# Performance work log

Hardware: AMD Instinct MI355X
Metric: run time of the kernel (lower is better)

## Reference

```python
import jax, jax.numpy as jnp
import numpy as np

B, IN, T, E, S, K, W, HD = 4096, 512, 10, 16, 2, 4, 1024, 64


def setup_inputs() -> dict:
    key = jax.random.key(0)
    ks = jax.random.split(key, 12)
    he = lambda k, shp, fan: jax.random.normal(k, shp, jnp.float32) * (2.0 / fan) ** 0.5
    x = jax.random.normal(ks[0], (B, IN + T), jnp.float32)
    return {
        'x': x,
        'gk': he(ks[1], (T, E), T),
        'rk0': he(ks[2], (E, IN, W), IN),
        'rb0': jax.random.normal(ks[3], (E, W), jnp.float32) * 0.01,
        'rk1': he(ks[4], (E, W, W), W),
        'rb1': jax.random.normal(ks[5], (E, W), jnp.float32) * 0.01,
        'sk0': he(ks[6], (S, IN, W), IN),
        'sb0': jax.random.normal(ks[7], (S, W), jnp.float32) * 0.01,
        'sk1': he(ks[8], (S, W, W), W),
        'sb1': jax.random.normal(ks[9], (S, W), jnp.float32) * 0.01,
        'hk': he(ks[10], (T, W, HD), W),
        'hb': jax.random.normal(ks[11], (T, HD), jnp.float32) * 0.01,
    }


def reference(x, gk, rk0, rb0, rk1, rb1, sk0, sb0, sk1, sb1, hk, hb):
    task_idx = x[:, -T:]            # (B, T) task one-hot / features
    feat = x[:, :-T]                # (B, IN)

    # --- top-k routing on task features ---
    gating_logits = task_idx @ gk                       # (B, E)
    topk_idx = jnp.argsort(-gating_logits, axis=-1)[:, :K]  # (B, K)
    topk_logits = jnp.take_along_axis(gating_logits, topk_idx, axis=-1)
    topk_weights = jax.nn.softmax(topk_logits, axis=-1)     # (B, K)

    # --- routed experts: run every expert chain densely, gather at the end ---
    # h: (B, E, d); each expert's independent MLP chain over the same input.
    h = jnp.broadcast_to(feat[:, None, :], (B, E, IN))
    h = jax.nn.relu(jnp.einsum('bei,eij->bej', h, rk0) + rb0[None])  # (B, E, W)
    h = jax.nn.relu(jnp.einsum('bei,eij->bej', h, rk1) + rb1[None])  # (B, E, W)
    h_sel = jnp.take_along_axis(h, topk_idx[:, :, None], axis=1)     # (B, K, W)
    routed = jnp.einsum('bkw,bk->bw', h_sel, topk_weights)           # (B, W)

    # --- shared experts: all run, mean-combined ---
    hs = jnp.broadcast_to(feat[:, None, :], (B, S, IN))
    hs = jax.nn.relu(jnp.einsum('bsi,sij->bsj', hs, sk0) + sb0[None])
    hs = jax.nn.relu(jnp.einsum('bsi,sij->bsj', hs, sk1) + sb1[None])
    shared = hs.mean(axis=1)                                         # (B, W)

    features_out = jnp.tanh(routed + shared)                         # (B, W)

    # --- per-task heads, select by task id ---
    heads_out = jnp.einsum('bw,twd->btd', features_out, hk) + hb[None]  # (B, T, HD)
    task_indices = task_idx.argmax(axis=-1)                             # (B,)
    out = jnp.take_along_axis(heads_out, task_indices[:, None, None], axis=1)[:, 0]
    return out
```

## Files before the change

kernel.cpp:

```cpp
#include <hip/hip_runtime.h>

typedef unsigned short u16;
typedef __attribute__((ext_vector_type(8))) short bf16x8;
typedef __attribute__((ext_vector_type(4))) float f32x4;

constexpr int B_ = 4096, IN_ = 512, T_ = 10, E_ = 16, S_ = 2, K_ = 4, W_ = 1024, HD_ = 64;
constexpr int XROW = IN_ + T_;
constexpr int NPAIR = B_ * (K_ + S_);
constexpr int MTU = 208;
constexpr int GEMM_GRID = MTU * 8;
constexpr int GB_ = 16;
constexpr int CB_GRID = 1034;


#define GLL16(g, l) __builtin_amdgcn_global_load_lds( \
    (const __attribute__((address_space(1))) void*)(g), \
    (__attribute__((address_space(3))) void*)(l), 16, 0, 0)

__device__ __forceinline__ u16 f2bf(float x) {
    unsigned u = __float_as_uint(x);
    return (u16)((u + 0x7fffu + ((u >> 16) & 1u)) >> 16);
}
__device__ __forceinline__ float bf2f(u16 b) { return __uint_as_float(((unsigned)b) << 16); }

__global__ __launch_bounds__(256) void featconv(const float* __restrict__ x, u16* __restrict__ featb) {
    int i = blockIdx.x * 256 + threadIdx.x;
    int b = i >> 8;
    int c2 = (i & 255) * 2;
    float2 v = *(const float2*)(x + (size_t)b * XROW + c2);
    ushort2 o;
    o.x = f2bf(v.x);
    o.y = f2bf(v.y);
    *(ushort2*)(featb + (size_t)b * IN_ + c2) = o;
}

__global__ __launch_bounds__(256) void gate_kernel(const float* __restrict__ x, const float* __restrict__ gk,
                                                   int* __restrict__ top4p, float* __restrict__ w6,
                                                   int* __restrict__ task_id, int* __restrict__ tpp,
                                                   int* __restrict__ bct_e, int* __restrict__ bct_t) {
    __shared__ float sgk[T_ * E_];
    __shared__ int hist[E_];
    __shared__ int thist[T_];
    int blk = blockIdx.x, tid = threadIdx.x;
    int b = blk * 256 + tid;
    if (tid < T_ * E_) sgk[tid] = gk[tid];
    if (tid < E_) hist[tid] = 0;
    if (tid < T_) thist[tid] = 0;
    __syncthreads();
    float tv[T_];
#pragma unroll
    for (int i = 0; i < T_; ++i) tv[i] = x[(size_t)b * XROW + IN_ + i];
    float lg[E_];
#pragma unroll
    for (int e = 0; e < E_; ++e) {
        float s = 0.f;
#pragma unroll
        for (int i = 0; i < T_; ++i) s += tv[i] * sgk[i * E_ + e];
        lg[e] = s;
    }
    int idx[K_]; float val[K_];
#pragma unroll
    for (int k = 0; k < K_; ++k) {
        int bi = 0; float bv = -1e30f;
#pragma unroll
        for (int e = 0; e < E_; ++e)
            if (lg[e] > bv) { bv = lg[e]; bi = e; }
        idx[k] = bi; val[k] = bv; lg[bi] = -1e30f;
    }
    float m = val[0];
    float ex[K_]; float s = 0.f;
#pragma unroll
    for (int k = 0; k < K_; ++k) { ex[k] = expf(val[k] - m); s += ex[k]; }
    float inv = 1.f / s;
#pragma unroll
    for (int k = 0; k < K_; ++k) {
        int lp = atomicAdd(&hist[idx[k]], 1);
        top4p[b * K_ + k] = idx[k] | (lp << 8);
        w6[b * 6 + k] = ex[k] * inv;
    }
    w6[b * 6 + 4] = 0.5f;
    w6[b * 6 + 5] = 0.5f;
    int ti = 0; float tb = tv[0];
#pragma unroll
    for (int i = 1; i < T_; ++i)
        if (tv[i] > tb) { tb = tv[i]; ti = i; }
    task_id[b] = ti;
    tpp[b] = atomicAdd(&thist[ti], 1);
    __syncthreads();
    if (tid < E_) bct_e[blk * E_ + tid] = hist[tid];
    if (tid < T_) bct_t[blk * T_ + tid] = thist[tid];
}

__global__ void build_tables(const int* __restrict__ bct_e, const int* __restrict__ bct_t,
                             int* __restrict__ meta, int* __restrict__ blockbase,
                             int* __restrict__ tblockbase) {
    __shared__ int cnt_s[E_], tcnt_s[T_], base_s[E_], pb_s[T_];
    int tid = threadIdx.x;
    if (tid < E_) {
        int s = 0;
        for (int blk = 0; blk < GB_; ++blk) s += bct_e[blk * E_ + tid];
        cnt_s[tid] = s;
        meta[tid] = s;
    }
    if (tid >= 32 && tid < 32 + T_) {
        int t = tid - 32;
        int s = 0;
        for (int blk = 0; blk < GB_; ++blk) s += bct_t[blk * T_ + t];
        tcnt_s[t] = s;
        meta[91 + t] = s;
    }
    __syncthreads();
    if (tid == 0) {
        int a = 0;
        for (int e = 0; e < E_; ++e) { base_s[e] = a; meta[16 + e] = a; a += cnt_s[e]; }
        int t = 0;
        for (int g = 0; g < 18; ++g) { meta[48 + g] = t; int c = (g < 16) ? cnt_s[g] : B_; t += (c + 127) >> 7; }
        meta[66] = t;
        int pr = 0, br = 0;
        for (int i = 0; i < T_; ++i) {
            pb_s[i] = pr;
            meta[70 + i] = pr;
            meta[80 + i] = br;
            pr += ((tcnt_s[i] + 3) >> 2) << 2;
            br += (tcnt_s[i] + 3) >> 2;
        }
        meta[90] = br;
    }
    __syncthreads();
    if (tid < E_) {
        int run = base_s[tid];
        for (int blk = 0; blk < GB_; ++blk) { blockbase[blk * E_ + tid] = run; run += bct_e[blk * E_ + tid]; }
    }
    if (tid >= 32 && tid < 32 + T_) {
        int t = tid - 32;
        int run = pb_s[t];
        for (int blk = 0; blk < GB_; ++blk) { tblockbase[blk * T_ + t] = run; run += bct_t[blk * T_ + t]; }
    }
}

__global__ __launch_bounds__(256) void scatter_kernel(const int* __restrict__ top4p,
                                                      const int* __restrict__ blockbase,
                                                      const int* __restrict__ task_id, const int* __restrict__ tpp,
                                                      const int* __restrict__ tblockbase,
                                                      int* __restrict__ pair_sample, int* __restrict__ pair_dst,
                                                      int* __restrict__ torder) {
    int blk = blockIdx.x, tid = threadIdx.x;
    int b = blk * 256 + tid;
#pragma unroll
    for (int k = 0; k < K_; ++k) {
        int v = top4p[b * K_ + k];
        int e = v & 0xFF, lp = v >> 8;
        int p = blockbase[blk * E_ + e] + lp;
        pair_sample[p] = b;
        pair_dst[p] = b * 6 + k;
    }
    pair_sample[B_ * K_ + b] = b;       pair_dst[B_ * K_ + b] = b * 6 + 4;
    pair_sample[B_ * K_ + B_ + b] = b;  pair_dst[B_ * K_ + B_ + b] = b * 6 + 5;
    torder[tblockbase[blk * T_ + task_id[b]] + tpp[b]] = b;
}

__global__ __launch_bounds__(256) void convbf16(const float* __restrict__ in, u16* __restrict__ out) {
    int i = blockIdx.x * 256 + threadIdx.x;
    float4 v = ((const float4*)in)[i];
    ushort4 o;
    o.x = f2bf(v.x); o.y = f2bf(v.y); o.z = f2bf(v.z); o.w = f2bf(v.w);
    ((ushort4*)out)[i] = o;
}

__global__ __launch_bounds__(256) void transconv3(const float* __restrict__ srcA, const float* __restrict__ srcB,
                                                  int splitZ, u16* __restrict__ out, int K, int N) {
    __shared__ float tile[64][33];
    int z = blockIdx.z;
    const float* src = (z < splitZ) ? (srcA + (size_t)z * K * N) : (srcB + (size_t)(z - splitZ) * K * N);
    int k0 = blockIdx.y * 64, n0 = blockIdx.x * 32;
    int tid = threadIdx.x;
    int r = tid >> 2, c8 = (tid & 3) * 8;
    const float* s0 = src + (size_t)(k0 + r) * N + n0 + c8;
    float4 v0 = *(const float4*)s0;
    float4 v1 = *(const float4*)(s0 + 4);
    tile[r][c8 + 0] = v0.x; tile[r][c8 + 1] = v0.y; tile[r][c8 + 2] = v0.z; tile[r][c8 + 3] = v0.w;
    tile[r][c8 + 4] = v1.x; tile[r][c8 + 5] = v1.y; tile[r][c8 + 6] = v1.z; tile[r][c8 + 7] = v1.w;
    __syncthreads();
    int n = tid >> 3, kc = (tid & 7) * 8;
    u16 o[8];
#pragma unroll
    for (int j = 0; j < 8; ++j) o[j] = f2bf(tile[kc + j][n]);
    *(bf16x8*)(out + (size_t)z * N * K + (size_t)(n0 + n) * K + k0 + kc) = *(const bf16x8*)o;
}

template <int K, int LAYER>
__global__ __launch_bounds__(256, 3) void gemm8(const u16* __restrict__ Asrc, const u16* __restrict__ wT,
                                                const float* __restrict__ rbias, const float* __restrict__ sbias,
                                                const int* __restrict__ pair_sample, const int* __restrict__ pair_dst,
                                                const int* __restrict__ meta, u16* __restrict__ outp) {
    __shared__ char lds[49152];
    const int* tpre = meta + 48;
    const int nwg = tpre[18] * 8;
    int p = blockIdx.x;
    if (p >= nwg) return;
    int q = nwg >> 3, r8 = nwg & 7;
    int xcd = p & 7, iofs = p >> 3;
    int lid = (xcd < r8 ? xcd * (q + 1) : r8 * (q + 1) + (xcd - r8) * q) + iofs;
    int mtu = lid >> 3, nt = lid & 7;
    int e = 0;
    while (mtu >= tpre[e + 1]) ++e;
    int mt = mtu - tpre[e];
    int off, cnt;
    if (e < E_) { off = meta[16 + e]; cnt = meta[e]; }
    else        { off = B_ * K_ + (e - E_) * B_; cnt = B_; }

    const int tid = threadIdx.x;
    const int srow = tid >> 2, sslot = tid & 3;
    const u16* wTe = wT + (size_t)e * W_ * K;
    const u16* ab[2];
    const u16* bb[2];
#pragma unroll
    for (int r = 0; r < 2; ++r) {
        int row = r * 64 + srow;
        int gchunk = sslot ^ ((row >> 1) & 3);
        int gm = mt * 128 + row;
        if (gm >= cnt) gm = cnt - 1;
        int arow = (LAYER == 1) ? pair_sample[off + gm] : (off + gm);
        ab[r] = Asrc + (size_t)arow * K + gchunk * 8;
        bb[r] = wTe + (size_t)(nt * 128 + row) * K + gchunk * 8;
    }

    auto STAGE = [&](int kt, int buf) {
        char* base = lds + buf * 16384;
        GLL16(ab[0] + kt * 32, base + tid * 16);
        GLL16(ab[1] + kt * 32, base + 4096 + tid * 16);
        GLL16(bb[0] + kt * 32, base + 8192 + tid * 16);
        GLL16(bb[1] + kt * 32, base + 12288 + tid * 16);
    };

    f32x4 acc[4][4];
#pragma unroll
    for (int i = 0; i < 4; ++i)
#pragma unroll
        for (int j = 0; j < 4; ++j) acc[i][j] = (f32x4){0.f, 0.f, 0.f, 0.f};

    const int lane = tid & 63, wid = tid >> 6;
    const int wr = wid >> 1, wc = wid & 1;
    const int fr = lane & 15;
    const int fkb = (lane >> 4) * 16;

    constexpr int NKT = K / 32;
    STAGE(0, 0);
    __builtin_amdgcn_sched_barrier(0);
    STAGE(1, 1);
    asm volatile("s_waitcnt vmcnt(4)" ::: "memory");
    __builtin_amdgcn_s_barrier();
    asm volatile("" ::: "memory");
    __builtin_amdgcn_sched_barrier(0);
    int rb = 0, sb = 2;
    for (int kt = 0; kt < NKT; ++kt) {
        if (kt + 2 < NKT) {
            STAGE(kt + 2, sb);
            sb = (sb == 2) ? 0 : sb + 1;
        }
        char* A = lds + rb * 16384;
        char* Bv = A + 8192;
        bf16x8 af[4], bf[4];
#pragma unroll
        for (int i = 0; i < 4; ++i) {
            int arow = wr * 64 + i * 16 + fr;
            af[i] = *(const bf16x8*)(A + arow * 64 + (fkb ^ (((arow >> 1) & 3) << 4)));
            int brow = wc * 64 + i * 16 + fr;
            bf[i] = *(const bf16x8*)(Bv + brow * 64 + (fkb ^ (((brow >> 1) & 3) << 4)));
        }
#pragma unroll
        for (int i = 0; i < 4; ++i)
#pragma unroll
            for (int j = 0; j < 4; ++j)
                acc[i][j] = __builtin_amdgcn_mfma_f32_16x16x32_bf16(af[i], bf[j], acc[i][j], 0, 0, 0);
        __builtin_amdgcn_sched_barrier(0);
        if (kt + 2 < NKT) {
            asm volatile("s_waitcnt vmcnt(4) lgkmcnt(0)" ::: "memory");
        } else {
            asm volatile("s_waitcnt vmcnt(0) lgkmcnt(0)" ::: "memory");
        }
        __builtin_amdgcn_s_barrier();
        asm volatile("" ::: "memory");
        __builtin_amdgcn_sched_barrier(0);
        rb = (rb == 2) ? 0 : rb + 1;
    }

    const float* bias = (e < E_) ? (rbias + (size_t)e * W_) : (sbias + (size_t)(e - E_) * W_);
#pragma unroll
    for (int i = 0; i < 4; ++i) {
#pragma unroll
        for (int reg = 0; reg < 4; ++reg) {
            int r = wr * 64 + i * 16 + (lane >> 4) * 4 + reg;
#pragma unroll
            for (int j = 0; j < 4; ++j) {
                int c = wc * 64 + j * 16 + fr;
                float v = acc[i][j][reg] + bias[nt * 128 + c];
                *(u16*)(lds + r * 256 + ((c * 2) ^ ((r & 7) << 4))) = f2bf(fmaxf(v, 0.f));
            }
        }
    }
    __syncthreads();
#pragma unroll
    for (int rr = 0; rr < 8; ++rr) {
        int flat = rr * 4096 + tid * 16;
        int r = flat >> 8;
        int co = flat & 255;
        int m = mt * 128 + r;
        if (m < cnt) {
            int outrow = (LAYER == 1) ? (off + m) : pair_dst[off + m];
            bf16x8 v = *(const bf16x8*)(lds + r * 256 + (co ^ ((r & 7) << 4)));
            *(bf16x8*)(outp + (size_t)outrow * W_ + nt * 128 + (co >> 1)) = v;
        }
    }
}

__global__ __launch_bounds__(256) void combine4(const u16* __restrict__ h2, const float* __restrict__ w6,
                                                const int* __restrict__ torder, const int* __restrict__ meta,
                                                const u16* __restrict__ hkb, const float* __restrict__ hb,
                                                float* __restrict__ out) {
    __shared__ float f[4][W_];
    __shared__ float partials[4][4][64];
    const int* bp = meta + 80;
    int blk = blockIdx.x;
    if (blk >= bp[T_]) return;
    int t = 0;
    while (blk >= bp[t + 1]) ++t;
    int slot0 = meta[70 + t] + (blk - bp[t]) * 4;
    int vend  = meta[70 + t] + meta[91 + t];
    int tid = threadIdx.x;
    int s0 = torder[slot0];
    int smp[4];
#pragma unroll
    for (int i = 0; i < 4; ++i) {
        int v = torder[slot0 + i];
        smp[i] = (slot0 + i < vend) ? v : s0;
    }
#pragma unroll
    for (int s = 0; s < 4; ++s) {
        int b = smp[s];
        float wsl[6];
#pragma unroll
        for (int qq = 0; qq < 6; ++qq) wsl[qq] = w6[b * 6 + qq];
        float sum[4] = {0.f, 0.f, 0.f, 0.f};
#pragma unroll
        for (int qq = 0; qq < 6; ++qq) {
            ushort4 v = *(const ushort4*)(h2 + (size_t)(b * 6 + qq) * W_ + tid * 4);
            sum[0] += wsl[qq] * bf2f(v.x);
            sum[1] += wsl[qq] * bf2f(v.y);
            sum[2] += wsl[qq] * bf2f(v.z);
            sum[3] += wsl[qq] * bf2f(v.w);
        }
        float4 tf;
        tf.x = tanhf(sum[0]); tf.y = tanhf(sum[1]); tf.z = tanhf(sum[2]); tf.w = tanhf(sum[3]);
        *(float4*)(&f[s][tid * 4]) = tf;
    }
    __syncthreads();
    int d = tid & 63, g = tid >> 6;
    const u16* hp = hkb + (size_t)t * W_ * HD_ + d;
    float acc[4] = {0.f, 0.f, 0.f, 0.f};
#pragma unroll 4
    for (int w = g; w < W_; w += 4) {
        float hv = bf2f(hp[(size_t)w * HD_]);
#pragma unroll
        for (int s = 0; s < 4; ++s) acc[s] += f[s][w] * hv;
    }
#pragma unroll
    for (int s = 0; s < 4; ++s) partials[g][s][d] = acc[s];
    __syncthreads();
    int ss = tid >> 6, dd = tid & 63;
    float r = partials[0][ss][dd] + partials[1][ss][dd] + partials[2][ss][dd] + partials[3][ss][dd]
            + hb[t * HD_ + dd];
    out[(size_t)smp[ss] * HD_ + dd] = r;
}

extern "C" void kernel_launch(void* const* d_in, const int* in_sizes, int n_in,
                              void* d_out, int out_size, void* d_ws, size_t ws_size,
                              hipStream_t stream) {
    const float* x   = (const float*)d_in[0];
    const float* gk  = (const float*)d_in[1];
    const float* rk0 = (const float*)d_in[2];
    const float* rb0 = (const float*)d_in[3];
    const float* rk1 = (const float*)d_in[4];
    const float* rb1 = (const float*)d_in[5];
    const float* sk0 = (const float*)d_in[6];
    const float* sb0 = (const float*)d_in[7];
    const float* sk1 = (const float*)d_in[8];
    const float* sb1 = (const float*)d_in[9];
    const float* hk  = (const float*)d_in[10];
    const float* hb  = (const float*)d_in[11];
    float* out = (float*)d_out;
    (void)in_sizes; (void)n_in; (void)out_size; (void)ws_size;

    char* ws = (char*)d_ws;
    size_t o = 0;
    auto alloc = [&](size_t bytes) { char* p = ws + o; o += (bytes + 255) & ~(size_t)255; return p; };
    int* meta        = (int*)alloc(512);
    int* bct_e       = (int*)alloc((size_t)GB_ * E_ * 4);
    int* bct_t       = (int*)alloc((size_t)GB_ * T_ * 4);
    int* blockbase   = (int*)alloc((size_t)GB_ * E_ * 4);
    int* tblockbase  = (int*)alloc((size_t)GB_ * T_ * 4);
    int* top4p       = (int*)alloc((size_t)B_ * K_ * 4);
    float* w6        = (float*)alloc((size_t)B_ * 6 * 4);
    int* task_id     = (int*)alloc((size_t)B_ * 4);
    int* tpp         = (int*)alloc((size_t)B_ * 4);
    int* pair_sample = (int*)alloc((size_t)NPAIR * 4);
    int* pair_dst    = (int*)alloc((size_t)NPAIR * 4);
    int* torder      = (int*)alloc((size_t)(B_ + 64) * 4);
    u16* featb       = (u16*)alloc((size_t)B_ * IN_ * 2);
    u16* w0T         = (u16*)alloc((size_t)(E_ + S_) * W_ * IN_ * 2);
    u16* w1T         = (u16*)alloc((size_t)(E_ + S_) * W_ * W_ * 2);
    u16* hkb         = (u16*)alloc((size_t)T_ * W_ * HD_ * 2);
    u16* h1          = (u16*)alloc((size_t)NPAIR * W_ * 2);
    u16* h2          = (u16*)alloc((size_t)NPAIR * W_ * 2);

    featconv<<<B_, 256, 0, stream>>>(x, featb);
    gate_kernel<<<GB_, 256, 0, stream>>>(x, gk, top4p, w6, task_id, tpp, bct_e, bct_t);
    build_tables<<<1, 64, 0, stream>>>(bct_e, bct_t, meta, blockbase, tblockbase);
    scatter_kernel<<<GB_, 256, 0, stream>>>(top4p, blockbase, task_id, tpp, tblockbase,
                                            pair_sample, pair_dst, torder);
    transconv3<<<dim3(W_ / 32, IN_ / 64, E_ + S_), 256, 0, stream>>>(rk0, sk0, E_, w0T, IN_, W_);
    transconv3<<<dim3(W_ / 32, W_ / 64, E_ + S_), 256, 0, stream>>>(rk1, sk1, E_, w1T, W_, W_);
    convbf16<<<(T_ * W_ * HD_) / 1024, 256, 0, stream>>>(hk, hkb);
    gemm8<IN_, 1><<<GEMM_GRID, 256, 0, stream>>>(featb, w0T, rb0, sb0, pair_sample, pair_dst, meta, h1);
    gemm8<W_, 2><<<GEMM_GRID, 256, 0, stream>>>(h1, w1T, rb1, sb1, pair_sample, pair_dst, meta, h2);
    combine4<<<CB_GRID, 256, 0, stream>>>(h2, w6, torder, meta, hkb, hb, out);
}
```

Before: 192.8 us.

## Restructure grouped GEMM pipelines for higher occupancy and use fast tanh

```diff
diff --git a/kernel.cpp b/kernel.cpp
--- a/kernel.cpp
+++ b/kernel.cpp
@@ -22,6 +22,11 @@
     return (u16)((u + 0x7fffu + ((u >> 16) & 1u)) >> 16);
 }
 __device__ __forceinline__ float bf2f(u16 b) { return __uint_as_float(((unsigned)b) << 16); }
+
+__device__ __forceinline__ float fast_tanh(float x) {
+    float t = __expf(2.f * x);
+    return 1.f - 2.f * __builtin_amdgcn_rcpf(t + 1.f);
+}
 
 __global__ __launch_bounds__(256) void featconv(const float* __restrict__ x, u16* __restrict__ featb) {
     int i = blockIdx.x * 256 + threadIdx.x;
@@ -189,11 +194,11 @@
 }
 
 template <int K, int LAYER>
-__global__ __launch_bounds__(256, 3) void gemm8(const u16* __restrict__ Asrc, const u16* __restrict__ wT,
+__global__ __launch_bounds__(256, 4) void gemm9(const u16* __restrict__ Asrc, const u16* __restrict__ wT,
                                                 const float* __restrict__ rbias, const float* __restrict__ sbias,
                                                 const int* __restrict__ pair_sample, const int* __restrict__ pair_dst,
                                                 const int* __restrict__ meta, u16* __restrict__ outp) {
-    __shared__ char lds[49152];
+    __shared__ char lds[32768];
     const int* tpre = meta + 48;
     const int nwg = tpre[18] * 8;
     int p = blockIdx.x;
@@ -246,19 +251,13 @@
 
     constexpr int NKT = K / 32;
     STAGE(0, 0);
-    __builtin_amdgcn_sched_barrier(0);
-    STAGE(1, 1);
-    asm volatile("s_waitcnt vmcnt(4)" ::: "memory");
+    asm volatile("s_waitcnt vmcnt(0)" ::: "memory");
     __builtin_amdgcn_s_barrier();
     asm volatile("" ::: "memory");
-    __builtin_amdgcn_sched_barrier(0);
-    int rb = 0, sb = 2;
+    int cur = 0;
     for (int kt = 0; kt < NKT; ++kt) {
-        if (kt + 2 < NKT) {
-            STAGE(kt + 2, sb);
-            sb = (sb == 2) ? 0 : sb + 1;
-        }
-        char* A = lds + rb * 16384;
+        if (kt + 1 < NKT) STAGE(kt + 1, cur ^ 1);
+        char* A = lds + cur * 16384;
         char* Bv = A + 8192;
         bf16x8 af[4], bf[4];
 #pragma unroll
@@ -273,16 +272,113 @@
 #pragma unroll
             for (int j = 0; j < 4; ++j)
                 acc[i][j] = __builtin_amdgcn_mfma_f32_16x16x32_bf16(af[i], bf[j], acc[i][j], 0, 0, 0);
-        __builtin_amdgcn_sched_barrier(0);
-        if (kt + 2 < NKT) {
-            asm volatile("s_waitcnt vmcnt(4) lgkmcnt(0)" ::: "memory");
-        } else {
-            asm volatile("s_waitcnt vmcnt(0) lgkmcnt(0)" ::: "memory");
-        }
+        asm volatile("s_waitcnt vmcnt(0) lgkmcnt(0)" ::: "memory");
         __builtin_amdgcn_s_barrier();
         asm volatile("" ::: "memory");
-        __builtin_amdgcn_sched_barrier(0);
-        rb = (rb == 2) ? 0 : rb + 1;
+        cur ^= 1;
+    }
+
+    const float* bias = (e < E_) ? (rbias + (size_t)e * W_) : (sbias + (size_t)(e - E_) * W_);
+#pragma unroll
+    for (int i = 0; i < 4; ++i) {
+#pragma unroll
+        for (int reg = 0; reg < 4; ++reg) {
+            int r = wr * 64 + i * 16 + (lane >> 4) * 4 + reg;
+#pragma unroll
+            for (int j = 0; j < 4; ++j) {
+                int c = wc * 64 + j * 16 + fr;
+                float v = acc[i][j][reg] + bias[nt * 128 + c];
+                *(u16*)(lds + r * 256 + ((c * 2) ^ ((r & 7) << 4))) = f2bf(fmaxf(v, 0.f));
+            }
+        }
+    }
+    __syncthreads();
+#pragma unroll
+    for (int rr = 0; rr < 8; ++rr) {
+        int flat = rr * 4096 + tid * 16;
+        int r = flat >> 8;
+        int co = flat & 255;
+        int m = mt * 128 + r;
+        if (m < cnt) {
+            int outrow = (LAYER == 1) ? (off + m) : pair_dst[off + m];
+            bf16x8 v = *(const bf16x8*)(lds + r * 256 + (co ^ ((r & 7) << 4)));
+            *(bf16x8*)(outp + (size_t)outrow * W_ + nt * 128 + (co >> 1)) = v;
+        }
+    }
+}
+
+template <int K, int LAYER>
+__global__ __launch_bounds__(256, 4) void gemm4(const u16* __restrict__ Asrc, const u16* __restrict__ wT,
+                                                const float* __restrict__ rbias, const float* __restrict__ sbias,
+                                                const int* __restrict__ pair_sample, const int* __restrict__ pair_dst,
+                                                const int* __restrict__ meta, u16* __restrict__ outp) {
+    __shared__ char lds[32768];
+    const int* tpre = meta + 48;
+    const int nwg = tpre[18] * 8;
+    int p = blockIdx.x;
+    if (p >= nwg) return;
+    int q = nwg >> 3, r8 = nwg & 7;
+    int xcd = p & 7, iofs = p >> 3;
+    int lid = (xcd < r8 ? xcd * (q + 1) : r8 * (q + 1) + (xcd - r8) * q) + iofs;
+    int mtu = lid >> 3, nt = lid & 7;
+    int e = 0;
+    while (mtu >= tpre[e + 1]) ++e;
+    int mt = mtu - tpre[e];
+    int off, cnt;
+    if (e < E_) { off = meta[16 + e]; cnt = meta[e]; }
+    else        { off = B_ * K_ + (e - E_) * B_; cnt = B_; }
+
+    const int tid = threadIdx.x;
+    const int srow = tid >> 3, sc = tid & 7;
+    const u16* wTe = wT + (size_t)e * W_ * K;
+    const u16* ab[4];
+    const u16* bb[4];
+#pragma unroll
+    for (int r = 0; r < 4; ++r) {
+        int row = r * 32 + srow;
+        int swz = (sc ^ (row & 7)) * 8;
+        int gm = mt * 128 + row;
+        if (gm >= cnt) gm = cnt - 1;
+        int arow = (LAYER == 1) ? pair_sample[off + gm] : (off + gm);
+        ab[r] = Asrc + (size_t)arow * K + swz;
+        bb[r] = wTe + (size_t)(nt * 128 + row) * K + swz;
+    }
+
+    f32x4 acc[4][4];
+#pragma unroll
+    for (int i = 0; i < 4; ++i)
+#pragma unroll
+        for (int j = 0; j < 4; ++j) acc[i][j] = (f32x4){0.f, 0.f, 0.f, 0.f};
+
+    const int lane = tid & 63, wid = tid >> 6;
+    const int wr = wid >> 1, wc = wid & 1;
+    const int fr = lane & 15;
+    const int fkb = (lane >> 4) * 16;
+
+    constexpr int NKT = K / 64;
+    for (int kt = 0; kt < NKT; ++kt) {
+#pragma unroll
+        for (int r = 0; r < 4; ++r) GLL16(ab[r] + kt * 64, lds + r * 4096 + tid * 16);
+#pragma unroll
+        for (int r = 0; r < 4; ++r) GLL16(bb[r] + kt * 64, lds + 16384 + r * 4096 + tid * 16);
+        __syncthreads();
+#pragma unroll
+        for (int kk = 0; kk < 2; ++kk) {
+            bf16x8 af[4], bf[4];
+#pragma unroll
+            for (int i = 0; i < 4; ++i) {
+                int arow = wr * 64 + i * 16 + fr;
+                af[i] = *(const bf16x8*)(lds + arow * 128 + ((kk * 64 + fkb) ^ ((arow & 7) << 4)));
+                int brow = wc * 64 + i * 16 + fr;
+                bf[i] = *(const bf16x8*)(lds + 16384 + brow * 128 + ((kk * 64 + fkb) ^ ((brow & 7) << 4)));
+            }
+#pragma unroll
+            for (int i = 0; i < 4; ++i)
+#pragma unroll
+                for (int j = 0; j < 4; ++j)
+                    acc[i][j] = __builtin_amdgcn_mfma_f32_16x16x32_bf16(af[i], bf[j], acc[i][j], 0, 0, 0);
+        }
+        __syncthreads();
     }
 
     const float* bias = (e < E_) ? (rbias + (size_t)e * W_) : (sbias + (size_t)(e - E_) * W_);
@@ -351,7 +447,8 @@
             sum[3] += wsl[qq] * bf2f(v.w);
         }
         float4 tf;
-        tf.x = tanhf(sum[0]); tf.y = tanhf(sum[1]); tf.z = tanhf(sum[2]); tf.w = tanhf(sum[3]);
+        tf.x = fast_tanh(sum[0]); tf.y = fast_tanh(sum[1]);
+        tf.z = fast_tanh(sum[2]); tf.w = fast_tanh(sum[3]);
         *(float4*)(&f[s][tid * 4]) = tf;
     }
     __syncthreads();
@@ -421,7 +518,7 @@
     transconv3<<<dim3(W_ / 32, IN_ / 64, E_ + S_), 256, 0, stream>>>(rk0, sk0, E_, w0T, IN_, W_);
     transconv3<<<dim3(W_ / 32, W_ / 64, E_ + S_), 256, 0, stream>>>(rk1, sk1, E_, w1T, W_, W_);
     convbf16<<<(T_ * W_ * HD_) / 1024, 256, 0, stream>>>(hk, hkb);
-    gemm8<IN_, 1><<<GEMM_GRID, 256, 0, stream>>>(featb, w0T, rb0, sb0, pair_sample, pair_dst, meta, h1);
-    gemm8<W_, 2><<<GEMM_GRID, 256, 0, stream>>>(h1, w1T, rb1, sb1, pair_sample, pair_dst, meta, h2);
+    gemm9<IN_, 1><<<GEMM_GRID, 256, 0, stream>>>(featb, w0T, rb0, sb0, pair_sample, pair_dst, meta, h1);
+    gemm4<W_, 2><<<GEMM_GRID, 256, 0, stream>>>(h1, w1T, rb1, sb1, pair_sample, pair_dst, meta, h2);
     combine4<<<CB_GRID, 256, 0, stream>>>(h2, w6, torder, meta, hkb, hb, out);
 }
```

Result: faster. 188.1 us (-2.4%).
